# Performance work log

Hardware: AMD Instinct MI355X
Metric: run time of the kernel (lower is better)

## Reference

```python
import jax, jax.numpy as jnp
import numpy as np

N = 50000
E = 800000
IN_DIM = 128
HID = 128
OUT_DIM = 128
H = 16
D = OUT_DIM // H  # head_dim = 8
EF = 4
RF = 20
KV_IN = 2 * IN_DIM + EF + RF  # 280
EPS = 1e-5


def _layernorm(x, w, b):
    mu = jnp.mean(x, axis=-1, keepdims=True)
    var = jnp.var(x, axis=-1, keepdims=True)
    return (x - mu) * jax.lax.rsqrt(var + EPS) * w + b


def _mlp(x, W1, b1, ln_w, ln_b, W2, b2):
    # Linear -> LayerNorm -> ReLU -> Linear (num_layer=2, norm=True)
    hdn = x @ W1 + b1
    hdn = jax.nn.relu(_layernorm(hdn, ln_w, ln_b))
    return hdn @ W2 + b2


def _lin_init(key, fan_in, fan_out):
    k1, k2 = jax.random.split(key)
    s = 1.0 / np.sqrt(fan_in)
    W = jax.random.uniform(k1, (fan_in, fan_out), jnp.float32, -s, s)
    b = jax.random.uniform(k2, (fan_out,), jnp.float32, -s, s)
    return W, b


def _mlp_params(key, in_dim, hid, out_dim):
    k1, k2 = jax.random.split(key)
    W1, b1 = _lin_init(k1, in_dim, hid)
    W2, b2 = _lin_init(k2, hid, out_dim)
    return W1, b1, jnp.ones((hid,), jnp.float32), jnp.zeros((hid,), jnp.float32), W2, b2


def setup_inputs() -> dict:
    key = jax.random.key(0)
    ks = jax.random.split(key, 10)
    h = jax.random.normal(ks[0], (N, IN_DIM), jnp.float32)
    rel_x = jax.random.normal(ks[1], (E, 3), jnp.float32)
    r_feat = jax.random.normal(ks[2], (E, RF), jnp.float32)
    edge_feat = jax.random.normal(ks[3], (E, EF), jnp.float32)
    edge_index = jax.random.randint(ks[4], (2, E), 0, N, jnp.int64)

    xk = _mlp_params(ks[5], KV_IN, HID, OUT_DIM)
    xv = _mlp_params(ks[6], KV_IN, HID, H)
    xq = _mlp_params(ks[7], IN_DIM, HID, OUT_DIM)
    ew_W, ew_b = _lin_init(ks[8], RF, 1)

    d = {"h": h, "rel_x": rel_x, "r_feat": r_feat, "edge_feat": edge_feat,
         "edge_index": edge_index, "ew_W": ew_W, "ew_b": ew_b}
    for name, p in (("xk", xk), ("xv", xv), ("xq", xq)):
        d[name + "_W1"], d[name + "_b1"], d[name + "_ln_w"], d[name + "_ln_b"], d[name + "_W2"], d[name + "_b2"] = p
    return d


def reference(h, rel_x, r_feat, edge_feat, edge_index,
              ew_W, ew_b,
              xk_W1, xk_b1, xk_ln_w, xk_ln_b, xk_W2, xk_b2,
              xv_W1, xv_b1, xv_ln_w, xv_ln_b, xv_W2, xv_b2,
              xq_W1, xq_b1, xq_ln_w, xq_ln_b, xq_W2, xq_b2):
    src, dst = edge_index[0], edge_index[1]
    hi = h[dst]  # [E, IN_DIM]
    hj = h[src]  # [E, IN_DIM]
    kv_input = jnp.concatenate([edge_feat, r_feat, hi, hj], axis=-1)  # [E, KV_IN]

    k = _mlp(kv_input, xk_W1, xk_b1, xk_ln_w, xk_ln_b, xk_W2, xk_b2).reshape(E, H, D)
    v = _mlp(kv_input, xv_W1, xv_b1, xv_ln_w, xv_ln_b, xv_W2, xv_b2)  # [E, H]
    e_w = jax.nn.sigmoid(r_feat @ ew_W + ew_b)  # [E, 1]
    v = (v * e_w)[:, :, None] * rel_x[:, None, :]  # [E, H, 3]

    q = _mlp(h, xq_W1, xq_b1, xq_ln_w, xq_ln_b, xq_W2, xq_b2).reshape(N, H, D)
    scores = jnp.sum(q[dst] * k, axis=-1) / np.sqrt(D)  # [E, H]

    # scatter_softmax over destination groups
    seg_max = jax.ops.segment_max(scores, dst, num_segments=N)  # [N, H]
    ex = jnp.exp(scores - seg_max[dst])
    denom = jax.ops.segment_sum(ex, dst, num_segments=N)  # [N, H]
    alpha = ex / denom[dst]  # [E, H]

    m = alpha[:, :, None] * v  # [E, H, 3]
    output = jax.ops.segment_sum(m, dst, num_segments=N)  # [N, H, 3]
    return output.mean(axis=1)  # [N, 3]
```

## Files before the change

kernel.cpp:

```cpp
#include <hip/hip_runtime.h>
#include <hip/hip_bf16.h>

#define NN 50000
#define EE 800000
#define ET 32
#define NT 16
#define QT 8
#define SCB 49

typedef unsigned int u32;
typedef __attribute__((ext_vector_type(8))) short short8;
typedef __attribute__((ext_vector_type(4))) float floatx4;

template<bool BF>
__device__ __forceinline__ float ldf(const void* p, int i){
  if constexpr (BF) return __bfloat162float(((const __hip_bfloat16*)p)[i]);
  else              return ((const float*)p)[i];
}
__device__ __forceinline__ int gidx(const int* ei, int pos, bool i64){
  return i64 ? ei[2*pos] : ei[pos];
}

__device__ __forceinline__ unsigned short f2bf(float f){
  u32 u = __float_as_uint(f);
  u32 r = u + 0x7FFFu + ((u>>16)&1u);
  return (unsigned short)(r>>16);
}
__device__ __forceinline__ float bf2f(unsigned short s){
  return __uint_as_float(((u32)s)<<16);
}

__global__ void k_detect(const u32* lnw, const u32* ei, int* flags){
  if (threadIdx.x == 0){
    flags[0] = (lnw[0] == 0x3F803F80u) ? 1 : 0;
    flags[1] = ((ei[1] | ei[3] | ei[5] | ei[7]) == 0u) ? 1 : 0;
  }
}

__global__ void __launch_bounds__(256)
k_hist(const int* ei, int* cnt, const int* flags){
  int t = blockIdx.x*256 + threadIdx.x;
  if (t >= EE) return;
  bool i64 = flags[1] != 0;
  atomicAdd(&cnt[gidx(ei, EE + t, i64)], 1);
}

__global__ void __launch_bounds__(256)
k_scan1(const int* cnt, int* bsum){
  __shared__ int wsum[4];
  int t=threadIdx.x, lane=t&63, wv=t>>6;
  int i0 = blockIdx.x*1024 + t*4;
  int s=0;
  #pragma unroll
  for(int j=0;j<4;j++){ int i=i0+j; s += (i<NN)?cnt[i]:0; }
  #pragma unroll
  for(int d=1;d<64;d<<=1) s += __shfl_xor(s,d);
  if(lane==0) wsum[wv]=s;
  __syncthreads();
  if(t==0) bsum[blockIdx.x]=wsum[0]+wsum[1]+wsum[2]+wsum[3];
}

__global__ void k_scan2(const int* bsum, int* bexcl, int* off){
  int lane=threadIdx.x;
  int v = (lane<SCB)?bsum[lane]:0;
  int sc=v;
  #pragma unroll
  for(int d=1;d<64;d<<=1){ int u=__shfl_up(sc,d); if(lane>=d) sc+=u; }
  if(lane<SCB) bexcl[lane]=sc-v;
  if(lane==63) off[NN]=sc;
}

__global__ void __launch_bounds__(256)
k_scan3(const int* cnt, const int* bexcl, int* off){
  __shared__ int wsum[4];
  int t=threadIdx.x, lane=t&63, wv=t>>6;
  int i0=blockIdx.x*1024 + t*4;
  int v0=(i0+0<NN)?cnt[i0+0]:0;
  int v1=(i0+1<NN)?cnt[i0+1]:0;
  int v2=(i0+2<NN)?cnt[i0+2]:0;
  int v3=(i0+3<NN)?cnt[i0+3]:0;
  int s=v0+v1+v2+v3;
  int sc=s;
  #pragma unroll
  for(int d=1;d<64;d<<=1){ int u=__shfl_up(sc,d); if(lane>=d) sc+=u; }
  if(lane==63) wsum[wv]=sc;
  __syncthreads();
  int base=bexcl[blockIdx.x];
  for(int k=0;k<wv;k++) base+=wsum[k];
  int excl=base+sc-s;
  if(i0+0<NN) off[i0+0]=excl;
  if(i0+1<NN) off[i0+1]=excl+v0;
  if(i0+2<NN) off[i0+2]=excl+v0+v1;
  if(i0+3<NN) off[i0+3]=excl+v0+v1+v2;
}

template<bool BF>
__device__ void scat_body(const int* ei, bool i64, const int* off, int* cur,
                          const void* rfeat, const void* relx,
                          const void* ewW, const void* ewb,
                          int* dsts, int* srcs, int* eperm,
                          float* relx_s, float* ews){
  int t = blockIdx.x*256 + threadIdx.x;
  if (t >= EE) return;
  int d = gidx(ei, EE + t, i64);
  int pos = off[d] + atomicAdd(&cur[d], 1);
  dsts[pos] = d;
  srcs[pos] = gidx(ei, t, i64);
  eperm[pos] = t;
  float aw = ldf<BF>(ewb, 0);
  #pragma unroll
  for (int j=0;j<20;j++) aw = fmaf(ldf<BF>(rfeat, t*20+j), ldf<BF>(ewW,j), aw);
  ews[pos] = (1.f/(1.f + expf(-aw))) * (1.f/16.f);
  relx_s[pos*3+0] = ldf<BF>(relx, t*3+0);
  relx_s[pos*3+1] = ldf<BF>(relx, t*3+1);
  relx_s[pos*3+2] = ldf<BF>(relx, t*3+2);
}
__global__ void __launch_bounds__(256)
k_scat(const int* ei, const int* off, int* cur,
       const void* rfeat, const void* relx, const void* ewW, const void* ewb,
       int* dsts, int* srcs, int* eperm, float* relx_s, float* ews, const int* flags){
  bool i64 = flags[1] != 0;
  if (flags[0]) scat_body<true >(ei,i64,off,cur,rfeat,relx,ewW,ewb,dsts,srcs,eperm,relx_s,ews);
  else          scat_body<false>(ei,i64,off,cur,rfeat,relx,ewW,ewb,dsts,srcs,eperm,relx_s,ews);
}

__global__ void __launch_bounds__(256)
k_wprep(const void* kW1, const void* vW1, const void* kW2, const void* vW2,
        unsigned short* w1sh, unsigned short* w1sl,
        unsigned short* w2kh, unsigned short* w2kl,
        unsigned short* w2vh, unsigned short* w2vl, const int* flags){
  int idx = blockIdx.x*256 + threadIdx.x;
  bool bf = flags[0] != 0;
  if (idx < 16384){ int c = idx>>7, k = idx&127;
    float f = bf ? __bfloat162float(((const __hip_bfloat16*)kW2)[k*128+c]) : ((const float*)kW2)[k*128+c];
    unsigned short h = f2bf(f); w2kh[idx]=h; w2kl[idx]=f2bf(f - bf2f(h)); }
  if (idx < 2048){ int c = idx>>7, k = idx&127;
    float f = bf ? __bfloat162float(((const __hip_bfloat16*)vW2)[k*16+c]) : ((const float*)vW2)[k*16+c];
    unsigned short h = f2bf(f); w2vh[idx]=h; w2vl[idx]=f2bf(f - bf2f(h)); }
  if (idx < 8192){ int c = idx>>5, k = idx&31;
    float f = 0.f;
    if (k < 24){
      if (c < 128) f = bf ? __bfloat162float(((const __hip_bfloat16*)kW1)[k*128+c]) : ((const float*)kW1)[k*128+c];
      else         f = bf ? __bfloat162float(((const __hip_bfloat16*)vW1)[k*128+(c-128)]) : ((const float*)vW1)[k*128+(c-128)];
    }
    unsigned short h = f2bf(f); w1sh[idx]=h; w1sl[idx]=f2bf(f - bf2f(h)); }
}

template<bool BF>
__device__ void node_body(const void* h, const void* kW1, const void* vW1,
                          float* hkd, float* hks, float* x){
  const int t  = threadIdx.x;
  const int n0 = blockIdx.x*NT;
  #pragma unroll
  for (int r=0;r<8;r++){ int idx=r*256+t; int n=idx>>7, j=idx&127;
    x[j*20+n] = ldf<BF>(h, (n0+n)*128 + j); }
  __syncthreads();
  const bool kb = (t < 128);
  const void* W = kb ? kW1 : vW1;
  const int  cc = kb ? t : t-128;
  float ad[NT], as[NT];
  #pragma unroll
  for (int e=0;e<NT;e++){ ad[e]=0.f; as[e]=0.f; }
  for (int j=0;j<128;j++){
    float wd = ldf<BF>(W, (24+j)*128 + cc);
    float ws = ldf<BF>(W, (152+j)*128 + cc);
    const float4* xr = (const float4*)&x[j*20];
    #pragma unroll
    for (int e4=0;e4<4;e4++){
      float4 xv = xr[e4];
      ad[e4*4+0]=fmaf(wd,xv.x,ad[e4*4+0]); as[e4*4+0]=fmaf(ws,xv.x,as[e4*4+0]);
      ad[e4*4+1]=fmaf(wd,xv.y,ad[e4*4+1]); as[e4*4+1]=fmaf(ws,xv.y,as[e4*4+1]);
      ad[e4*4+2]=fmaf(wd,xv.z,ad[e4*4+2]); as[e4*4+2]=fmaf(ws,xv.z,as[e4*4+2]);
      ad[e4*4+3]=fmaf(wd,xv.w,ad[e4*4+3]); as[e4*4+3]=fmaf(ws,xv.w,as[e4*4+3]);
    }
  }
  #pragma unroll
  for (int e=0;e<NT;e++){
    hkd[(n0+e)*256 + t] = ad[e];
    hks[(n0+e)*256 + t] = as[e];
  }
}
__global__ void __launch_bounds__(256)
k_node(const void* h, const void* kW1, const void* vW1, float* hkd, float* hks, const int* flags){
  __shared__ float x[128*20];
  if (flags[0]) node_body<true >(h,kW1,vW1,hkd,hks,x);
  else          node_body<false>(h,kW1,vW1,hkd,hks,x);
}

template<bool BF>
__device__ void q_body(const void* h, const void* W1, const void* b1,
                       const void* lnw, const void* lnb,
                       const void* W2, const void* b2, float* qws,
                       float* x, float* y, float2* redp, float* mus, float* scs){
  const int t = threadIdx.x, c = t&127, half = t>>7;
  const int n0 = blockIdx.x*QT;
  #pragma unroll
  for (int r=0;r<4;r++){ int idx=r*256+t; int n=idx>>7, j=idx&127;
    x[j*12+n] = ldf<BF>(h, (n0+n)*128 + j); }
  __syncthreads();
  float a[4];
  { float bb = ldf<BF>(b1,c);
    #pragma unroll
    for (int r=0;r<4;r++) a[r]=bb; }
  for (int j=0;j<128;j++){
    float w = ldf<BF>(W1, j*128+c);
    float4 xv = *(const float4*)&x[j*12 + half*4];
    a[0]=fmaf(w,xv.x,a[0]); a[1]=fmaf(w,xv.y,a[1]);
    a[2]=fmaf(w,xv.z,a[2]); a[3]=fmaf(w,xv.w,a[3]);
  }
  #pragma unroll
  for (int r=0;r<4;r++) y[(half*4+r)*128 + c] = a[r];
  __syncthreads();
  { int p=t>>5, l32=t&31;
    float s=0.f,s2=0.f;
    #pragma unroll
    for (int k=0;k<4;k++){ float v=y[p*128 + l32 + 32*k]; s+=v; s2=fmaf(v,v,s2); }
    redp[t]=make_float2(s,s2); }
  __syncthreads();
  if (t<QT){
    float s=0.f,s2=0.f;
    for (int i=0;i<32;i++){ float2 f=redp[t*32+i]; s+=f.x; s2+=f.y; }
    float mu=s*(1.f/128.f), var=s2*(1.f/128.f)-mu*mu;
    mus[t]=mu; scs[t]=rsqrtf(var+1e-5f);
  }
  __syncthreads();
  { float lw=ldf<BF>(lnw,c), lb=ldf<BF>(lnb,c);
    #pragma unroll
    for (int r=0;r<4;r++){ int row=half*4+r;
      float v=(a[r]-mus[row])*scs[row]*lw+lb;
      y[row*128+c]=fmaxf(v,0.f); } }
  __syncthreads();
  float o[4];
  { float bb=ldf<BF>(b2,c);
    #pragma unroll
    for (int r=0;r<4;r++) o[r]=bb; }
  for (int j4=0;j4<32;j4++){
    float w0=ldf<BF>(W2,(j4*4+0)*128+c);
    float w1=ldf<BF>(W2,(j4*4+1)*128+c);
    float w2=ldf<BF>(W2,(j4*4+2)*128+c);
    float w3=ldf<BF>(W2,(j4*4+3)*128+c);
    #pragma unroll
    for (int r=0;r<4;r++){
      float4 xv=*(const float4*)&y[(half*4+r)*128 + j4*4];
      o[r]=fmaf(w0,xv.x,o[r]); o[r]=fmaf(w1,xv.y,o[r]);
      o[r]=fmaf(w2,xv.z,o[r]); o[r]=fmaf(w3,xv.w,o[r]);
    }
  }
  #pragma unroll
  for (int r=0;r<4;r++) qws[(n0+half*4+r)*128 + c] = o[r];
}
__global__ void __launch_bounds__(256)
k_q(const void* h, const void* W1, const void* b1, const void* lnw, const void* lnb,
    const void* W2, const void* b2, float* qws, const int* flags){
  __shared__ float x[128*12];
  __shared__ float y[QT*128];
  __shared__ float2 redp[256];
  __shared__ float mus[QT], scs[QT];
  if (flags[0]) q_body<true >(h,W1,b1,lnw,lnb,W2,b2,qws,x,y,redp,mus,scs);
  else          q_body<false>(h,W1,b1,lnw,lnb,W2,b2,qws,x,y,redp,mus,scs);
}

template<bool BF>
__device__ void edge_body(const void* rfeat, const void* efeat,
                          const int* dsts, const int* srcs, const int* eperm,
                          const void* kb1, const void* vb1,
                          const void* klnw, const void* klnb,
                          const void* vlnw, const void* vlnb,
                          const void* kb2, const void* vb2,
                          const unsigned short* w1sh, const unsigned short* w1sl,
                          const unsigned short* w2kh, const unsigned short* w2kl,
                          const unsigned short* w2vh, const unsigned short* w2vl,
                          const float* hkd, const float* hks, const float* qws,
                          const float* ews, float* scw, float* vsw,
                          unsigned short* ahi, unsigned short* sfh,
                          int* dste, int* srce, float* ewv,
                          float2 (*lnred)[4], float* sc_lds){
  const int t  = threadIdx.x;
  const int e0 = blockIdx.x*ET;
  const int lane = t&63, w = t>>6;
  const int arow = lane&15, agrp = lane>>4;

  if (t < ET)             dste[t]    = dsts[e0+t];
  else if (t < 2*ET)      srce[t-ET] = srcs[e0+(t-ET)];
  else if (t < 3*ET)      ewv[t-2*ET] = ews[e0+(t-2*ET)];
  #pragma unroll
  for (int it=0; it<4; it++){
    int id = it*256+t; int e = id>>5, j = id&31;
    int ge = eperm[e0+e];
    float f = (j<4) ? ldf<BF>(efeat, ge*4+j)
            : (j<24 ? ldf<BF>(rfeat, ge*20+(j-4)) : 0.f);
    sfh[e*40+j] = f2bf(f);
  }
  __syncthreads();

  const int wcol = w*64 + arow;
  float b1c[4];
  #pragma unroll
  for (int nt=0; nt<4; nt++){ int col = wcol + nt*16;
    b1c[nt] = (col<128) ? ldf<BF>(kb1,col) : ldf<BF>(vb1,col-128); }
  floatx4 C[2][4];
  #pragma unroll
  for (int g=0; g<2; g++){
    #pragma unroll
    for (int r=0;r<4;r++){
      int e = g*16 + agrp*4 + r;
      const float* bd = hkd + (u32)dste[e]*256u + wcol;
      const float* bs = hks + (u32)srce[e]*256u + wcol;
      #pragma unroll
      for (int nt=0; nt<4; nt++)
        C[g][nt][r] = bd[nt*16] + bs[nt*16] + b1c[nt];
    }
  }
  #pragma unroll
  for (int g=0; g<2; g++){
    short8 Ah = *(const short8*)&sfh[(g*16+arow)*40 + agrp*8];
    #pragma unroll
    for (int nt=0; nt<4; nt++){
      const int col = wcol + nt*16;
      short8 Bh = *(const short8*)&w1sh[col*32 + agrp*8];
      short8 Bl = *(const short8*)&w1sl[col*32 + agrp*8];
      C[g][nt] = __builtin_amdgcn_mfma_f32_16x16x32_bf16(Ah, Bh, C[g][nt], 0,0,0);
      C[g][nt] = __builtin_amdgcn_mfma_f32_16x16x32_bf16(Ah, Bl, C[g][nt], 0,0,0);
    }
  }
  #pragma unroll
  for (int g=0; g<2; g++){
    float s1[4], s2[4];
    #pragma unroll
    for (int r=0;r<4;r++){ s1[r]=0.f; s2[r]=0.f; }
    #pragma unroll
    for (int nt=0; nt<4; nt++)
      #pragma unroll
      for (int r=0;r<4;r++){ float v=C[g][nt][r]; s1[r]+=v; s2[r]=fmaf(v,v,s2[r]); }
    #pragma unroll
    for (int d=1; d<16; d<<=1){
      #pragma unroll
      for (int r=0;r<4;r++){ s1[r]+=__shfl_xor(s1[r],d); s2[r]+=__shfl_xor(s2[r],d); }
    }
    if (arow==0){
      #pragma unroll
      for (int r=0;r<4;r++) lnred[g*16+agrp*4+r][w] = make_float2(s1[r], s2[r]);
    }
  }
  __syncthreads();
  float mu[2][4], rs[2][4];
  { int b = w>>1;
    #pragma unroll
    for (int g=0; g<2; g++)
      #pragma unroll
      for (int r=0;r<4;r++){
        int row = g*16+agrp*4+r;
        float2 p0 = lnred[row][2*b], p1 = lnred[row][2*b+1];
        float s = p0.x+p1.x, q = p0.y+p1.y;
        float m = s*(1.f/128.f);
        mu[g][r]=m; rs[g][r]=rsqrtf(q*(1.f/128.f) - m*m + 1e-5f);
      }
  }
  #pragma unroll
  for (int nt=0; nt<4; nt++){
    const int col = wcol + nt*16;
    const bool kb = (col<128); const int cc = kb?col:col-128;
    float lw = kb?ldf<BF>(klnw,cc):ldf<BF>(vlnw,cc);
    float lb = kb?ldf<BF>(klnb,cc):ldf<BF>(vlnb,cc);
    #pragma unroll
    for (int g=0; g<2; g++){
      #pragma unroll
      for (int r=0;r<4;r++){
        int row = g*16+agrp*4+r;
        float v = (C[g][nt][r]-mu[g][r])*rs[g][r]*lw + lb;
        v = fmaxf(v, 0.f);
        int idx = (row*256 + col) ^ ((row&7)<<3);
        ahi[idx] = f2bf(v);
      }
    }
  }
  __syncthreads();

  const int c0 = (2*w+0)*16 + arow;
  const int c1 = (2*w+1)*16 + arow;
  floatx4 Ck[2][2], Cv;
  { float b0=ldf<BF>(kb2,c0), b1v=ldf<BF>(kb2,c1);
    #pragma unroll
    for (int g=0;g<2;g++)
      #pragma unroll
      for (int r=0;r<4;r++){ Ck[g][0][r]=b0; Ck[g][1][r]=b1v; } }
  const bool dov = (w&1);
  const int  gv  = w>>1;
  if (dov){ float bv=ldf<BF>(vb2,arow);
    #pragma unroll
    for (int r=0;r<4;r++) Cv[r]=bv; }
  #pragma unroll
  for (int ks=0; ks<4; ks++){
    short8 B0h = *(const short8*)&w2kh[c0*128 + ks*32 + agrp*8];
    short8 B0l = *(const short8*)&w2kl[c0*128 + ks*32 + agrp*8];
    short8 B1h = *(const short8*)&w2kh[c1*128 + ks*32 + agrp*8];
    short8 B1l = *(const short8*)&w2kl[c1*128 + ks*32 + agrp*8];
    #pragma unroll
    for (int g=0; g<2; g++){
      int aidx = ((g*16+arow)*256 + ks*32 + agrp*8) ^ ((arow&7)<<3);
      short8 Ah = *(const short8*)&ahi[aidx];
      Ck[g][0] = __builtin_amdgcn_mfma_f32_16x16x32_bf16(Ah, B0h, Ck[g][0], 0,0,0);
      Ck[g][0] = __builtin_amdgcn_mfma_f32_16x16x32_bf16(Ah, B0l, Ck[g][0], 0,0,0);
      Ck[g][1] = __builtin_amdgcn_mfma_f32_16x16x32_bf16(Ah, B1h, Ck[g][1], 0,0,0);
      Ck[g][1] = __builtin_amdgcn_mfma_f32_16x16x32_bf16(Ah, B1l, Ck[g][1], 0,0,0);
    }
    if (dov){
      int avidx = ((gv*16+arow)*256 + 128 + ks*32 + agrp*8) ^ ((arow&7)<<3);
      short8 Avh = *(const short8*)&ahi[avidx];
      short8 Bvh = *(const short8*)&w2vh[arow*128 + ks*32 + agrp*8];
      short8 Bvl = *(const short8*)&w2vl[arow*128 + ks*32 + agrp*8];
      Cv = __builtin_amdgcn_mfma_f32_16x16x32_bf16(Avh, Bvh, Cv, 0,0,0);
      Cv = __builtin_amdgcn_mfma_f32_16x16x32_bf16(Avh, Bvl, Cv, 0,0,0);
    }
  }
  if (dov){
    #pragma unroll
    for (int r=0;r<4;r++){
      int row = gv*16 + agrp*4 + r;
      vsw[(size_t)(e0+row)*16 + arow] = Cv[r]*ewv[row];
    }
  }
  #pragma unroll
  for (int g=0; g<2; g++){
    float p0[4], p1[4];
    #pragma unroll
    for (int r=0;r<4;r++){
      int e = g*16 + agrp*4 + r;
      const float* qr = qws + (u32)dste[e]*128u;
      p0[r] = qr[c0]*Ck[g][0][r];
      p1[r] = qr[c1]*Ck[g][1][r];
    }
    #pragma unroll
    for (int d=1; d<8; d<<=1){
      #pragma unroll
      for (int r=0;r<4;r++){ p0[r]+=__shfl_xor(p0[r],d); p1[r]+=__shfl_xor(p1[r],d); }
    }
    int j = arow&7;
    float val = (j<4) ? ((j&2)?((j&1)?p0[3]:p0[2]):((j&1)?p0[1]:p0[0]))
                      : ((j&2)?((j&1)?p1[3]:p1[2]):((j&1)?p1[1]:p1[0]));
    int e  = g*16 + agrp*4 + (j&3);
    int hh = (j<4) ? (4*w + (arow>>3)) : (4*w + 2 + (arow>>3));
    sc_lds[e*17 + hh] = val*0.35355339059327373f;
  }
  __syncthreads();
  #pragma unroll
  for (int u=0; u<2; u++){
    int idx = u*256 + t;
    scw[(size_t)e0*16 + idx] = sc_lds[(idx>>4)*17 + (idx&15)];
  }
}
__global__ void __launch_bounds__(256)
k_edge(const void* rfeat, const void* efeat,
       const int* dsts, const int* srcs, const int* eperm,
       const void* kb1, const void* vb1,
       const void* klnw, const void* klnb, const void* vlnw, const void* vlnb,
       const void* kb2, const void* vb2,
       const unsigned short* w1sh, const unsigned short* w1sl,
       const unsigned short* w2kh, const unsigned short* w2kl,
       const unsigned short* w2vh, const unsigned short* w2vl,
       const float* hkd, const float* hks, const float* qws,
       const float* ews, float* scw, float* vsw, const int* flags){
  __shared__ unsigned short ahi[ET*256];
  __shared__ unsigned short sfh[ET*40];
  __shared__ int   dste[ET], srce[ET];
  __shared__ float ewv[ET];
  __shared__ float2 lnred[ET][4];
  __shared__ float sc_lds[ET*17];
  if (flags[0]) edge_body<true >(rfeat,efeat,dsts,srcs,eperm,kb1,vb1,klnw,klnb,vlnw,vlnb,kb2,vb2,
                                 w1sh,w1sl,w2kh,w2kl,w2vh,w2vl,hkd,hks,qws,ews,scw,vsw,
                                 ahi,sfh,dste,srce,ewv,lnred,sc_lds);
  else          edge_body<false>(rfeat,efeat,dsts,srcs,eperm,kb1,vb1,klnw,klnb,vlnw,vlnb,kb2,vb2,
                                 w1sh,w1sl,w2kh,w2kl,w2vh,w2vl,hkd,hks,qws,ews,scw,vsw,
                                 ahi,sfh,dste,srce,ewv,lnred,sc_lds);
}

template<bool BF>
__device__ void soft_body(const int* off, const float* relx_s,
                          const float* scw, const float* vsw, void* dout){
  const int t=threadIdx.x, lane=t&63, wv=t>>6;
  const int n = blockIdx.x*4 + wv;
  const int lo=off[n], hi=off[n+1];
  if (lo>=hi){
    if (lane<3){
      if constexpr (BF) ((__hip_bfloat16*)dout)[n*3+lane]=__float2bfloat16(0.f);
      else              ((float*)dout)[n*3+lane]=0.f;
    }
    return;
  }
  const int h=lane&15, es=lane>>4;
  float m=-3.4e38f;
  for (int p=lo+es; p<hi; p+=4) m = fmaxf(m, scw[(size_t)p*16+h]);
  m = fmaxf(m, __shfl_xor(m,16));
  m = fmaxf(m, __shfl_xor(m,32));
  float den=0.f, t0=0.f, t1=0.f, t2=0.f;
  for (int p=lo+es; p<hi; p+=4){
    float ex = expf(scw[(size_t)p*16+h]-m);
    den += ex;
    float a = ex * vsw[(size_t)p*16+h];
    float r0=relx_s[p*3+0], r1=relx_s[p*3+1], r2=relx_s[p*3+2];
    t0 = fmaf(a,r0,t0); t1 = fmaf(a,r1,t1); t2 = fmaf(a,r2,t2);
  }
  den += __shfl_xor(den,16);
  den += __shfl_xor(den,32);
  float id = 1.f/den;
  t0*=id; t1*=id; t2*=id;
  #pragma unroll
  for (int d=1; d<64; d<<=1){
    t0+=__shfl_xor(t0,d); t1+=__shfl_xor(t1,d); t2+=__shfl_xor(t2,d);
  }
  if (lane==0){
    if constexpr (BF){
      ((__hip_bfloat16*)dout)[n*3+0]=__float2bfloat16(t0);
      ((__hip_bfloat16*)dout)[n*3+1]=__float2bfloat16(t1);
      ((__hip_bfloat16*)dout)[n*3+2]=__float2bfloat16(t2);
    } else {
      ((float*)dout)[n*3+0]=t0;
      ((float*)dout)[n*3+1]=t1;
      ((float*)dout)[n*3+2]=t2;
    }
  }
}
__global__ void __launch_bounds__(256)
k_soft(const int* off, const float* relx_s,
       const float* scw, const float* vsw, void* dout, const int* flags){
  if (flags[0]) soft_body<true >(off,relx_s,scw,vsw,dout);
  else          soft_body<false>(off,relx_s,scw,vsw,dout);
}

extern "C" void kernel_launch(void* const* d_in, const int* in_sizes, int n_in,
                              void* d_out, int out_size, void* d_ws, size_t ws_size,
                              hipStream_t stream){
  const void* h     = d_in[0];
  const void* relx  = d_in[1];
  const void* rfeat = d_in[2];
  const void* efeat = d_in[3];
  const int*  ei    = (const int*)d_in[4];
  const void* ewW   = d_in[5];
  const void* ewb   = d_in[6];
  const void* kW1 = d_in[7],  *kb1 = d_in[8],  *klnw = d_in[9],  *klnb = d_in[10], *kW2 = d_in[11], *kb2 = d_in[12];
  const void* vW1 = d_in[13], *vb1 = d_in[14], *vlnw = d_in[15], *vlnb = d_in[16], *vW2 = d_in[17], *vb2 = d_in[18];
  const void* qW1 = d_in[19], *qb1 = d_in[20], *qlnw = d_in[21], *qlnb = d_in[22], *qW2 = d_in[23], *qb2 = d_in[24];

  float* qws = (float*)d_ws;
  float* hkd = qws + (size_t)NN*128;
  float* hks = hkd + (size_t)NN*256;
  float* scw = hks + (size_t)NN*256;
  float* vsw = scw + (size_t)EE*16;
  float* relx_s = vsw + (size_t)EE*16;
  float* ews = relx_s + (size_t)EE*3;
  int*   cnt = (int*)(ews + EE);
  int*   cur = cnt + NN;
  int*   off = cur + NN;
  int*  dsts = off + NN + 64;
  int*  srcs = dsts + EE;
  int* eperm = srcs + EE;
  unsigned short* w1sh = (unsigned short*)(eperm + EE);
  unsigned short* w1sl = w1sh + 8192;
  unsigned short* w2kh = w1sl + 8192;
  unsigned short* w2kl = w2kh + 16384;
  unsigned short* w2vh = w2kl + 16384;
  unsigned short* w2vl = w2vh + 2048;
  int* bsum  = (int*)(w2vl + 2048);
  int* bexcl = bsum + 64;
  int* flags = bexcl + 64;

  hipMemsetAsync(cnt, 0, (size_t)2*NN*sizeof(int), stream);
  k_detect<<<1, 64, 0, stream>>>((const u32*)klnw, (const u32*)ei, flags);
  k_hist<<<(EE+255)/256, 256, 0, stream>>>(ei, cnt, flags);
  k_scan1<<<SCB, 256, 0, stream>>>(cnt, bsum);
  k_scan2<<<1, 64, 0, stream>>>(bsum, bexcl, off);
  k_scan3<<<SCB, 256, 0, stream>>>(cnt, bexcl, off);
  k_scat<<<(EE+255)/256, 256, 0, stream>>>(ei, off, cur, rfeat, relx, ewW, ewb,
                                           dsts, srcs, eperm, relx_s, ews, flags);
  k_wprep<<<64, 256, 0, stream>>>(kW1, vW1, kW2, vW2, w1sh, w1sl, w2kh, w2kl, w2vh, w2vl, flags);
  k_node<<<NN/NT, 256, 0, stream>>>(h, kW1, vW1, hkd, hks, flags);
  k_q<<<NN/QT, 256, 0, stream>>>(h, qW1, qb1, qlnw, qlnb, qW2, qb2, qws, flags);
  k_edge<<<EE/ET, 256, 0, stream>>>(rfeat, efeat, dsts, srcs, eperm,
                                    kb1, vb1, klnw, klnb, vlnw, vlnb, kb2, vb2,
                                    w1sh, w1sl, w2kh, w2kl, w2vh, w2vl,
                                    hkd, hks, qws, ews, scw, vsw, flags);
  k_soft<<<(NN+3)/4, 256, 0, stream>>>(off, relx_s, scw, vsw, d_out, flags);
}
```

Before: 878.0 us.

## Use split-bf16 MFMA for node projection and move edge staging into registers

The node kernel's per-node projection of h through the first-layer kv weights was a scalar fp32 FMA loop. It now uses 16x16x32 bf16 MFMA with a hi/lo split on both operands (three MFMAs per tile) to keep near-fp32 accuracy. New pre-split weight buffers are built in the weight-prep kernel, which now launches more blocks. In the edge kernel, the dst/src indices and the small edge-feature A operand are loaded straight into registers instead of staged through LDS, which drops one barrier. LayerNorm output is now packed with the v_cvt_pk_bf16_f32 instruction.

```diff
diff --git a/kernel.cpp b/kernel.cpp
--- a/kernel.cpp
+++ b/kernel.cpp
@@ -4,7 +4,6 @@
 #define NN 50000
 #define EE 800000
 #define ET 32
-#define NT 16
 #define QT 8
 #define SCB 49
 
@@ -28,6 +27,11 @@
 }
 __device__ __forceinline__ float bf2f(unsigned short s){
   return __uint_as_float(((u32)s)<<16);
+}
+__device__ __forceinline__ u32 cvtpk(float lo, float hi){
+  u32 r;
+  asm("v_cvt_pk_bf16_f32 %0, %1, %2" : "=v"(r) : "v"(lo), "v"(hi));
+  return r;
 }
 
 __global__ void k_detect(const u32* lnw, const u32* ei, int* flags){
@@ -127,10 +131,19 @@
 __global__ void __launch_bounds__(256)
 k_wprep(const void* kW1, const void* vW1, const void* kW2, const void* vW2,
         unsigned short* w1sh, unsigned short* w1sl,
+        unsigned short* w1nh, unsigned short* w1nl,
         unsigned short* w2kh, unsigned short* w2kl,
         unsigned short* w2vh, unsigned short* w2vl, const int* flags){
   int idx = blockIdx.x*256 + threadIdx.x;
   bool bf = flags[0] != 0;
+  {
+    int c = idx>>7, k = idx&127;
+    int row = (c<256) ? (24+k) : (152+k);
+    int cc  = c & 127;
+    const void* W = ((c&255)<128) ? kW1 : vW1;
+    float f = bf ? __bfloat162float(((const __hip_bfloat16*)W)[row*128+cc]) : ((const float*)W)[row*128+cc];
+    unsigned short h = f2bf(f); w1nh[idx]=h; w1nl[idx]=f2bf(f - bf2f(h));
+  }
   if (idx < 16384){ int c = idx>>7, k = idx&127;
     float f = bf ? __bfloat162float(((const __hip_bfloat16*)kW2)[k*128+c]) : ((const float*)kW2)[k*128+c];
     unsigned short h = f2bf(f); w2kh[idx]=h; w2kl[idx]=f2bf(f - bf2f(h)); }
@@ -147,44 +160,72 @@
 }
 
 template<bool BF>
-__device__ void node_body(const void* h, const void* kW1, const void* vW1,
-                          float* hkd, float* hks, float* x){
-  const int t  = threadIdx.x;
-  const int n0 = blockIdx.x*NT;
-  #pragma unroll
-  for (int r=0;r<8;r++){ int idx=r*256+t; int n=idx>>7, j=idx&127;
-    x[j*20+n] = ldf<BF>(h, (n0+n)*128 + j); }
-  __syncthreads();
-  const bool kb = (t < 128);
-  const void* W = kb ? kW1 : vW1;
-  const int  cc = kb ? t : t-128;
-  float ad[NT], as[NT];
-  #pragma unroll
-  for (int e=0;e<NT;e++){ ad[e]=0.f; as[e]=0.f; }
-  for (int j=0;j<128;j++){
-    float wd = ldf<BF>(W, (24+j)*128 + cc);
-    float ws = ldf<BF>(W, (152+j)*128 + cc);
-    const float4* xr = (const float4*)&x[j*20];
-    #pragma unroll
-    for (int e4=0;e4<4;e4++){
-      float4 xv = xr[e4];
-      ad[e4*4+0]=fmaf(wd,xv.x,ad[e4*4+0]); as[e4*4+0]=fmaf(ws,xv.x,as[e4*4+0]);
-      ad[e4*4+1]=fmaf(wd,xv.y,ad[e4*4+1]); as[e4*4+1]=fmaf(ws,xv.y,as[e4*4+1]);
-      ad[e4*4+2]=fmaf(wd,xv.z,ad[e4*4+2]); as[e4*4+2]=fmaf(ws,xv.z,as[e4*4+2]);
-      ad[e4*4+3]=fmaf(wd,xv.w,ad[e4*4+3]); as[e4*4+3]=fmaf(ws,xv.w,as[e4*4+3]);
-    }
-  }
-  #pragma unroll
-  for (int e=0;e<NT;e++){
-    hkd[(n0+e)*256 + t] = ad[e];
-    hks[(n0+e)*256 + t] = as[e];
-  }
-}
-__global__ void __launch_bounds__(256)
-k_node(const void* h, const void* kW1, const void* vW1, float* hkd, float* hks, const int* flags){
-  __shared__ float x[128*20];
-  if (flags[0]) node_body<true >(h,kW1,vW1,hkd,hks,x);
-  else          node_body<false>(h,kW1,vW1,hkd,hks,x);
+__device__ void node_body(const void* h, const unsigned short* w1nh, const unsigned short* w1nl,
+                          float* hkd, float* hks, unsigned short* xh, unsigned short* xl){
+  const int t = threadIdx.x;
+  const int n0 = blockIdx.x*16;
+  const int lane = t&63, w = t>>6;
+  const int arow = lane&15, agrp = lane>>4;
+  { int nd = t>>4, c8 = (t&15)*8;
+    float v[8];
+    if constexpr (!BF){
+      float4 a = *(const float4*)&((const float*)h)[(n0+nd)*128 + c8];
+      float4 b = *(const float4*)&((const float*)h)[(n0+nd)*128 + c8 + 4];
+      v[0]=a.x; v[1]=a.y; v[2]=a.z; v[3]=a.w; v[4]=b.x; v[5]=b.y; v[6]=b.z; v[7]=b.w;
+    } else {
+      short8 raw = *(const short8*)&((const __hip_bfloat16*)h)[(n0+nd)*128 + c8];
+      #pragma unroll
+      for (int i=0;i<8;i++) v[i] = bf2f((unsigned short)raw[i]);
+    }
+    short8 hv, lv;
+    #pragma unroll
+    for (int i=0;i<8;i++){
+      unsigned short hh = f2bf(v[i]);
+      hv[i] = (short)hh; lv[i] = (short)f2bf(v[i]-bf2f(hh));
+    }
+    int sidx = (nd*128 + c8) ^ ((nd&7)<<3);
+    *(short8*)&xh[sidx] = hv;
+    *(short8*)&xl[sidx] = lv;
+  }
+  __syncthreads();
+  floatx4 acc[8];
+  #pragma unroll
+  for (int ct=0; ct<8; ct++)
+    #pragma unroll
+    for (int r=0;r<4;r++) acc[ct][r]=0.f;
+  #pragma unroll
+  for (int ks=0; ks<4; ks++){
+    int aidx = (arow*128 + ks*32 + agrp*8) ^ ((arow&7)<<3);
+    short8 Ah = *(const short8*)&xh[aidx];
+    short8 Al = *(const short8*)&xl[aidx];
+    #pragma unroll
+    for (int ct=0; ct<8; ct++){
+      int gc = w*128 + ct*16 + arow;
+      short8 Bh = *(const short8*)&w1nh[gc*128 + ks*32 + agrp*8];
+      short8 Bl = *(const short8*)&w1nl[gc*128 + ks*32 + agrp*8];
+      acc[ct] = __builtin_amdgcn_mfma_f32_16x16x32_bf16(Ah, Bh, acc[ct], 0,0,0);
+      acc[ct] = __builtin_amdgcn_mfma_f32_16x16x32_bf16(Al, Bh, acc[ct], 0,0,0);
+      acc[ct] = __builtin_amdgcn_mfma_f32_16x16x32_bf16(Ah, Bl, acc[ct], 0,0,0);
+    }
+  }
+  #pragma unroll
+  for (int ct=0; ct<8; ct++){
+    int gc = w*128 + ct*16 + arow;
+    float* dst = (gc<256) ? (hkd + (size_t)0) : (hks - 256);
+    #pragma unroll
+    for (int r=0;r<4;r++){
+      int n = n0 + agrp*4 + r;
+      dst[(size_t)n*256 + gc] = acc[ct][r];
+    }
+  }
+}
+__global__ void __launch_bounds__(256)
+k_node(const void* h, const unsigned short* w1nh, const unsigned short* w1nl,
+       float* hkd, float* hks, const int* flags){
+  __shared__ unsigned short xh[16*128];
+  __shared__ unsigned short xl[16*128];
+  if (flags[0]) node_body<true >(h,w1nh,w1nl,hkd,hks,xh,xl);
+  else          node_body<false>(h,w1nh,w1nl,hkd,hks,xh,xl);
 }
 
 template<bool BF>
@@ -272,26 +313,37 @@
                           const unsigned short* w2vh, const unsigned short* w2vl,
                           const float* hkd, const float* hks, const float* qws,
                           const float* ews, float* scw, float* vsw,
-                          unsigned short* ahi, unsigned short* sfh,
-                          int* dste, int* srce, float* ewv,
-                          float2 (*lnred)[4], float* sc_lds){
+                          unsigned short* ahi, float2 (*lnred)[4], float* sc_lds){
   const int t  = threadIdx.x;
   const int e0 = blockIdx.x*ET;
   const int lane = t&63, w = t>>6;
   const int arow = lane&15, agrp = lane>>4;
 
-  if (t < ET)             dste[t]    = dsts[e0+t];
-  else if (t < 2*ET)      srce[t-ET] = srcs[e0+(t-ET)];
-  else if (t < 3*ET)      ewv[t-2*ET] = ews[e0+(t-2*ET)];
-  #pragma unroll
-  for (int it=0; it<4; it++){
-    int id = it*256+t; int e = id>>5, j = id&31;
-    int ge = eperm[e0+e];
-    float f = (j<4) ? ldf<BF>(efeat, ge*4+j)
-            : (j<24 ? ldf<BF>(rfeat, ge*20+(j-4)) : 0.f);
-    sfh[e*40+j] = f2bf(f);
-  }
-  __syncthreads();
+  int dste[2][4], srce[2][4];
+  #pragma unroll
+  for (int g=0; g<2; g++)
+    #pragma unroll
+    for (int r=0;r<4;r++){
+      int e = e0 + g*16 + agrp*4 + r;
+      dste[g][r] = dsts[e];
+      srce[g][r] = srcs[e];
+    }
+
+  short8 A0, A1;
+  #pragma unroll
+  for (int i=0;i<8;i++){ A0[i]=0; A1[i]=0; }
+  if (agrp < 3){
+    int ge0 = eperm[e0 + arow];
+    int ge1 = eperm[e0 + 16 + arow];
+    #pragma unroll
+    for (int i=0;i<8;i++){
+      int j = agrp*8 + i;
+      float f0 = (j<4) ? ldf<BF>(efeat, ge0*4+j) : ldf<BF>(rfeat, ge0*20+(j-4));
+      float f1 = (j<4) ? ldf<BF>(efeat, ge1*4+j) : ldf<BF>(rfeat, ge1*20+(j-4));
+      A0[i] = (short)f2bf(f0);
+      A1[i] = (short)f2bf(f1);
+    }
+  }
 
   const int wcol = w*64 + arow;
   float b1c[4];
@@ -303,25 +355,22 @@
   for (int g=0; g<2; g++){
     #pragma unroll
     for (int r=0;r<4;r++){
-      int e = g*16 + agrp*4 + r;
-      const float* bd = hkd + (u32)dste[e]*256u + wcol;
-      const float* bs = hks + (u32)srce[e]*256u + wcol;
+      const float* bd = hkd + (u32)dste[g][r]*256u + wcol;
+      const float* bs = hks + (u32)srce[g][r]*256u + wcol;
       #pragma unroll
       for (int nt=0; nt<4; nt++)
         C[g][nt][r] = bd[nt*16] + bs[nt*16] + b1c[nt];
     }
   }
   #pragma unroll
-  for (int g=0; g<2; g++){
-    short8 Ah = *(const short8*)&sfh[(g*16+arow)*40 + agrp*8];
-    #pragma unroll
-    for (int nt=0; nt<4; nt++){
-      const int col = wcol + nt*16;
-      short8 Bh = *(const short8*)&w1sh[col*32 + agrp*8];
-      short8 Bl = *(const short8*)&w1sl[col*32 + agrp*8];
-      C[g][nt] = __builtin_amdgcn_mfma_f32_16x16x32_bf16(Ah, Bh, C[g][nt], 0,0,0);
-      C[g][nt] = __builtin_amdgcn_mfma_f32_16x16x32_bf16(Ah, Bl, C[g][nt], 0,0,0);
-    }
+  for (int nt=0; nt<4; nt++){
+    const int col = wcol + nt*16;
+    short8 Bh = *(const short8*)&w1sh[col*32 + agrp*8];
+    short8 Bl = *(const short8*)&w1sl[col*32 + agrp*8];
+    C[0][nt] = __builtin_amdgcn_mfma_f32_16x16x32_bf16(A0, Bh, C[0][nt], 0,0,0);
+    C[0][nt] = __builtin_amdgcn_mfma_f32_16x16x32_bf16(A0, Bl, C[0][nt], 0,0,0);
+    C[1][nt] = __builtin_amdgcn_mfma_f32_16x16x32_bf16(A1, Bh, C[1][nt], 0,0,0);
+    C[1][nt] = __builtin_amdgcn_mfma_f32_16x16x32_bf16(A1, Bl, C[1][nt], 0,0,0);
   }
   #pragma unroll
   for (int g=0; g<2; g++){
@@ -364,14 +413,17 @@
     float lb = kb?ldf<BF>(klnb,cc):ldf<BF>(vlnb,cc);
     #pragma unroll
     for (int g=0; g<2; g++){
-      #pragma unroll
-      for (int r=0;r<4;r++){
-        int row = g*16+agrp*4+r;
-        float v = (C[g][nt][r]-mu[g][r])*rs[g][r]*lw + lb;
-        v = fmaxf(v, 0.f);
-        int idx = (row*256 + col) ^ ((row&7)<<3);
-        ahi[idx] = f2bf(v);
-      }
+      float v[4];
+      #pragma unroll
+      for (int r=0;r<4;r++)
+        v[r] = fmaxf((C[g][nt][r]-mu[g][r])*rs[g][r]*lw + lb, 0.f);
+      u32 p01 = cvtpk(v[0], v[1]);
+      u32 p23 = cvtpk(v[2], v[3]);
+      int row0 = g*16 + agrp*4;
+      ahi[((row0+0)*256 + col) ^ (((row0+0)&7)<<3)] = (unsigned short)p01;
+      ahi[((row0+1)*256 + col) ^ (((row0+1)&7)<<3)] = (unsigned short)(p01>>16);
+      ahi[((row0+2)*256 + col) ^ (((row0+2)&7)<<3)] = (unsigned short)p23;
+      ahi[((row0+3)*256 + col) ^ (((row0+3)&7)<<3)] = (unsigned short)(p23>>16);
     }
   }
   __syncthreads();
@@ -417,7 +469,7 @@
     #pragma unroll
     for (int r=0;r<4;r++){
       int row = gv*16 + agrp*4 + r;
-      vsw[(size_t)(e0+row)*16 + arow] = Cv[r]*ewv[row];
+      vsw[(size_t)(e0+row)*16 + arow] = Cv[r]*ews[e0+row];
     }
   }
   #pragma unroll
@@ -425,8 +477,7 @@
     float p0[4], p1[4];
     #pragma unroll
     for (int r=0;r<4;r++){
-      int e = g*16 + agrp*4 + r;
-      const float* qr = qws + (u32)dste[e]*128u;
+      const float* qr = qws + (u32)dste[g][r]*128u;
       p0[r] = qr[c0]*Ck[g][0][r];
       p1[r] = qr[c1]*Ck[g][1][r];
     }
@@ -461,17 +512,14 @@
        const float* hkd, const float* hks, const float* qws,
        const float* ews, float* scw, float* vsw, const int* flags){
   __shared__ unsigned short ahi[ET*256];
-  __shared__ unsigned short sfh[ET*40];
-  __shared__ int   dste[ET], srce[ET];
-  __shared__ float ewv[ET];
   __shared__ float2 lnred[ET][4];
   __shared__ float sc_lds[ET*17];
   if (flags[0]) edge_body<true >(rfeat,efeat,dsts,srcs,eperm,kb1,vb1,klnw,klnb,vlnw,vlnb,kb2,vb2,
                                  w1sh,w1sl,w2kh,w2kl,w2vh,w2vl,hkd,hks,qws,ews,scw,vsw,
-                                 ahi,sfh,dste,srce,ewv,lnred,sc_lds);
+                                 ahi,lnred,sc_lds);
   else          edge_body<false>(rfeat,efeat,dsts,srcs,eperm,kb1,vb1,klnw,klnb,vlnw,vlnb,kb2,vb2,
                                  w1sh,w1sl,w2kh,w2kl,w2vh,w2vl,hkd,hks,qws,ews,scw,vsw,
-                                 ahi,sfh,dste,srce,ewv,lnred,sc_lds);
+                                 ahi,lnred,sc_lds);
 }
 
 template<bool BF>
@@ -556,7 +604,9 @@
   int* eperm = srcs + EE;
   unsigned short* w1sh = (unsigned short*)(eperm + EE);
   unsigned short* w1sl = w1sh + 8192;
-  unsigned short* w2kh = w1sl + 8192;
+  unsigned short* w1nh = w1sl + 8192;
+  unsigned short* w1nl = w1nh + 65536;
+  unsigned short* w2kh = w1nl + 65536;
   unsigned short* w2kl = w2kh + 16384;
   unsigned short* w2vh = w2kl + 16384;
   unsigned short* w2vl = w2vh + 2048;
@@ -572,8 +622,9 @@
   k_scan3<<<SCB, 256, 0, stream>>>(cnt, bexcl, off);
   k_scat<<<(EE+255)/256, 256, 0, stream>>>(ei, off, cur, rfeat, relx, ewW, ewb,
                                            dsts, srcs, eperm, relx_s, ews, flags);
-  k_wprep<<<64, 256, 0, stream>>>(kW1, vW1, kW2, vW2, w1sh, w1sl, w2kh, w2kl, w2vh, w2vl, flags);
-  k_node<<<NN/NT, 256, 0, stream>>>(h, kW1, vW1, hkd, hks, flags);
+  k_wprep<<<256, 256, 0, stream>>>(kW1, vW1, kW2, vW2, w1sh, w1sl, w1nh, w1nl,
+                                   w2kh, w2kl, w2vh, w2vl, flags);
+  k_node<<<NN/16, 256, 0, stream>>>(h, w1nh, w1nl, hkd, hks, flags);
   k_q<<<NN/QT, 256, 0, stream>>>(h, qW1, qb1, qlnw, qlnb, qW2, qb2, qws, flags);
   k_edge<<<EE/ET, 256, 0, stream>>>(rfeat, efeat, dsts, srcs, eperm,
                                     kb1, vb1, klnw, klnb, vlnw, vlnb, kb2, vb2,
```

Measured after the change: 962.3 us. 9.6% more time.
